# Kernel optimization log

Hardware: AMD Instinct MI355X
Metric: run time of the kernel (lower is better)

## Reference

```python
import jax, jax.numpy as jnp
import numpy as np

VERTICES = np.array([[-1.0, -1.0, 1.0], [-1.0, 1.0, 1.0], [1.0, 1.0, 1.0], [1.0, -1.0, 1.0]], dtype=np.float32)  # [4,3]


def _gather2d(img, yi, xi):
    # img: [C,IH,IW], yi/xi: [OH,OW] int32 -> [C,OH,OW]
    return img[:, yi, xi]


def _grid_sample_bilinear_zero(inp, grid):
    # inp: [B,C,IH,IW], grid: [B,OH,OW,2] in [-1,1] (x,y), align_corners=True (old torch semantics)
    B, C, IH, IW = inp.shape
    gx = grid[..., 0]
    gy = grid[..., 1]
    ix = (gx + 1.0) * (IW - 1) * 0.5
    iy = (gy + 1.0) * (IH - 1) * 0.5
    x0 = jnp.floor(ix)
    y0 = jnp.floor(iy)
    x1 = x0 + 1.0
    y1 = y0 + 1.0
    wx1 = ix - x0  # frac weights
    wy1 = iy - y0
    wx0 = 1.0 - wx1
    wy0 = 1.0 - wy1

    def corner(xf, yf, w):
        inb = ((xf >= 0) & (xf <= IW - 1) & (yf >= 0) & (yf <= IH - 1)).astype(inp.dtype)
        xi = jnp.clip(xf, 0, IW - 1).astype(jnp.int32)
        yi = jnp.clip(yf, 0, IH - 1).astype(jnp.int32)
        vals = jax.vmap(_gather2d)(inp, yi, xi)  # [B,C,OH,OW]
        return vals * (w * inb)[:, None, :, :]

    out = (corner(x0, y0, wx0 * wy0) + corner(x1, y0, wx1 * wy0)
           + corner(x0, y1, wx0 * wy1) + corner(x1, y1, wx1 * wy1))
    return out


def affine_spatial_transform(inp, theta, OH, OW):
    B, C, IH, IW = inp.shape
    hs = jnp.linspace(-1.0, 1.0, OH)
    ws = jnp.linspace(-1.0, 1.0, OW)
    hh = jnp.broadcast_to(hs[:, None], (OH, OW))
    ww = jnp.broadcast_to(ws[None, :], (OH, OW))
    t = jnp.stack([ww, hh, jnp.ones((OH, OW), dtype=inp.dtype)], axis=2)  # [OH,OW,3]
    # source_grid = theta @ t : [B,OH,OW,2]
    grid = jnp.einsum('bij,hwj->bhwi', theta, t)
    out = _grid_sample_bilinear_zero(inp, grid)
    v = jnp.asarray(VERTICES)  # [4,3]
    vout = jnp.einsum('bij,vj->bvi', theta, v)  # [B,4,2]
    x_coord = (vout[..., 0] + 1.0) * IW * 0.5
    y_coord = (vout[..., 1] + 1.0) * IH * 0.5
    vertices_out = jnp.stack([x_coord, y_coord], axis=2)  # [B,4,2]
    return out, vertices_out


def setup_inputs() -> dict:
    key = jax.random.key(0)
    k1, k2 = jax.random.split(key)
    B, C, IH, IW = 16, 64, 256, 256
    inp = jax.random.normal(k1, (B, C, IH, IW), dtype=jnp.float32)
    theta = jax.random.normal(k2, (B, 2, 3), dtype=jnp.float32)
    return {"input": inp, "theta": theta, "OH": 256, "OW": 256}


def reference(input, theta, OH, OW):
    return affine_spatial_transform(input, theta, OH, OW)
```

## Files before the change

kernel.cpp:

```cpp
#include <hip/hip_runtime.h>

#define B  16
#define C  64
#define IH 256
#define IW 256
#define OH 256
#define OW 256

#define TW 16
#define TH 16
#define CC 16
#define NWT (OW / TW)
#define NHT (OH / TH)
#define NCC (C / CC)
#define NB  (B * NCC * NHT * NWT)

typedef float f2 __attribute__((ext_vector_type(2)));
typedef f2 __attribute__((aligned(4))) f2u;

__global__ __launch_bounds__(256) void ast_fused(const float* __restrict__ inp,
                                                 const float* __restrict__ theta,
                                                 float* __restrict__ out) {
    if (blockIdx.x == 0 && threadIdx.x < B * 4) {
        const int tid = threadIdx.x;
        const int b = tid >> 2;
        const int v = tid & 3;
        const float vx_tab[4] = {-1.0f, -1.0f, 1.0f, 1.0f};
        const float vy_tab[4] = {-1.0f,  1.0f, 1.0f, -1.0f};
        const float Vx = vx_tab[v];
        const float Vy = vy_tab[v];
        const float ox = theta[b*6+0]*Vx + theta[b*6+1]*Vy + theta[b*6+2];
        const float oy = theta[b*6+3]*Vx + theta[b*6+4]*Vy + theta[b*6+5];
        float* vo = out + (size_t)B * C * OH * OW;
        vo[b*8 + v*2 + 0] = (ox + 1.0f) * ((float)IW * 0.5f);
        vo[b*8 + v*2 + 1] = (oy + 1.0f) * ((float)IH * 0.5f);
    }

    int id = (int)blockIdx.x;
    id = (id & 7) * (NB >> 3) + (id >> 3);

    const int wt = id & (NWT - 1); id >>= 4;
    const int ht = id & (NHT - 1); id >>= 4;
    const int b  = id & (B - 1);   id >>= 4;
    const int cc = id;

    const int tx = threadIdx.x & (TW - 1);
    const int ty = threadIdx.x >> 4;
    const int w = wt * TW + tx;
    const int h = ht * TH + ty;

    const float wn = -1.0f + (2.0f / (float)(OW - 1)) * (float)w;
    const float hn = -1.0f + (2.0f / (float)(OH - 1)) * (float)h;

    const float t00 = theta[b*6+0], t01 = theta[b*6+1], t02 = theta[b*6+2];
    const float t10 = theta[b*6+3], t11 = theta[b*6+4], t12 = theta[b*6+5];

    const float gx = t00 * wn + t01 * hn + t02;
    const float gy = t10 * wn + t11 * hn + t12;

    const float ix = (gx + 1.0f) * ((float)(IW - 1) * 0.5f);
    const float iy = (gy + 1.0f) * ((float)(IH - 1) * 0.5f);

    const float x0f = floorf(ix);
    const float y0f = floorf(iy);

    const float wx1 = ix - x0f;
    const float wy1 = iy - y0f;
    const float wx0 = 1.0f - wx1;
    const float wy0 = 1.0f - wy1;

    const bool inx0 = (x0f >= 0.0f) && (x0f <= (float)(IW - 1));
    const bool inx1 = (x0f + 1.0f >= 0.0f) && (x0f + 1.0f <= (float)(IW - 1));
    const bool iny0 = (y0f >= 0.0f) && (y0f <= (float)(IH - 1));
    const bool iny1 = (y0f + 1.0f >= 0.0f) && (y0f + 1.0f <= (float)(IH - 1));

    const float w00 = (inx0 && iny0) ? wx0 * wy0 : 0.0f;
    const float w10 = (inx1 && iny0) ? wx1 * wy0 : 0.0f;
    const float w01 = (inx0 && iny1) ? wx0 * wy1 : 0.0f;
    const float w11 = (inx1 && iny1) ? wx1 * wy1 : 0.0f;

    const int  basex = (int)fminf(fmaxf(x0f, 0.0f), (float)(IW - 2));
    const bool selA  = (x0f <= (float)(IW - 2));
    const bool selB  = (x0f >= 0.0f);

    const int y0 = (int)fminf(fmaxf(y0f,        0.0f), (float)(IH - 1));
    const int y1 = (int)fminf(fmaxf(y0f + 1.0f, 0.0f), (float)(IH - 1));

    const int off0 = y0 * IW + basex;
    const int off1 = y1 * IW + basex;

    const bool any_in = (inx0 || inx1) && (iny0 || iny1);

    const int c0 = cc * CC;
    const float* __restrict__ p = inp + ((size_t)b * C + c0) * (IH * IW);
    float* __restrict__ o = out + (((size_t)b * C + c0) * OH + h) * OW + w;

    if (any_in) {
        #pragma unroll 16
        for (int c = 0; c < CC; ++c) {
            const f2 ra = *(const f2u*)(p + off0);
            const f2 rb = *(const f2u*)(p + off1);
            const float a00 = selA ? ra.x : ra.y;
            const float a10 = selB ? ra.y : ra.x;
            const float b00 = selA ? rb.x : rb.y;
            const float b11 = selB ? rb.y : rb.x;
            float v = w00 * a00;
            v = fmaf(w10, a10, v);
            v = fmaf(w01, b00, v);
            v = fmaf(w11, b11, v);
            __builtin_nontemporal_store(v, o);
            p += IH * IW;
            o += OH * OW;
        }
    } else {
        #pragma unroll 16
        for (int c = 0; c < CC; ++c) {
            __builtin_nontemporal_store(0.0f, o);
            o += OH * OW;
        }
    }
}

extern "C" void kernel_launch(void* const* d_in, const int* in_sizes, int n_in,
                              void* d_out, int out_size, void* d_ws, size_t ws_size,
                              hipStream_t stream) {
    const float* inp   = (const float*)d_in[0];
    const float* theta = (const float*)d_in[1];
    float* out = (float*)d_out;

    ast_fused<<<NB, 256, 0, stream>>>(inp, theta, out);
}
```

Measured before the change: 495.9 us.

## Stage per-tile source bounding box in LDS across all channels with double buffering

Each block now covers one 16x16 output tile for all 64 channels. It computes the source-space bounding box of the tile's corners, cooperatively loads that box per channel into XOR-swizzled double-buffered shared memory with register prefetch of the next channel, and then does the bilinear gathers from LDS. Tiles whose box lies fully outside the image write zeros with an early return, and boxes too large for LDS fall back to direct global gathers. This is meant to replace scattered global gathers with coalesced loads, at the cost of one __syncthreads per channel, fewer blocks, and extra loads when the box is much larger than the tile footprint.

After: 609.1 us. +22.8%, slower.

```diff
diff --git a/kernel.cpp b/kernel.cpp
--- a/kernel.cpp
+++ b/kernel.cpp
@@ -9,61 +9,57 @@
 
 #define TW 16
 #define TH 16
-#define CC 16
 #define NWT (OW / TW)
 #define NHT (OH / TH)
-#define NCC (C / CC)
-#define NB  (B * NCC * NHT * NWT)
-
-typedef float f2 __attribute__((ext_vector_type(2)));
-typedef f2 __attribute__((aligned(4))) f2u;
+#define NB  (B * NHT * NWT)
+#define CAP 4096
+
+typedef float f4 __attribute__((ext_vector_type(4)));
 
 __global__ __launch_bounds__(256) void ast_fused(const float* __restrict__ inp,
                                                  const float* __restrict__ theta,
                                                  float* __restrict__ out) {
-    if (blockIdx.x == 0 && threadIdx.x < B * 4) {
-        const int tid = threadIdx.x;
-        const int b = tid >> 2;
-        const int v = tid & 3;
+    const int tid = threadIdx.x;
+
+    if (blockIdx.x == 0 && tid < B * 4) {
+        const int b_ = tid >> 2;
+        const int v  = tid & 3;
         const float vx_tab[4] = {-1.0f, -1.0f, 1.0f, 1.0f};
         const float vy_tab[4] = {-1.0f,  1.0f, 1.0f, -1.0f};
         const float Vx = vx_tab[v];
         const float Vy = vy_tab[v];
-        const float ox = theta[b*6+0]*Vx + theta[b*6+1]*Vy + theta[b*6+2];
-        const float oy = theta[b*6+3]*Vx + theta[b*6+4]*Vy + theta[b*6+5];
+        const float ox = theta[b_*6+0]*Vx + theta[b_*6+1]*Vy + theta[b_*6+2];
+        const float oy = theta[b_*6+3]*Vx + theta[b_*6+4]*Vy + theta[b_*6+5];
         float* vo = out + (size_t)B * C * OH * OW;
-        vo[b*8 + v*2 + 0] = (ox + 1.0f) * ((float)IW * 0.5f);
-        vo[b*8 + v*2 + 1] = (oy + 1.0f) * ((float)IH * 0.5f);
+        vo[b_*8 + v*2 + 0] = (ox + 1.0f) * ((float)IW * 0.5f);
+        vo[b_*8 + v*2 + 1] = (oy + 1.0f) * ((float)IH * 0.5f);
     }
 
     int id = (int)blockIdx.x;
     id = (id & 7) * (NB >> 3) + (id >> 3);
 
-    const int wt = id & (NWT - 1); id >>= 4;
-    const int ht = id & (NHT - 1); id >>= 4;
-    const int b  = id & (B - 1);   id >>= 4;
-    const int cc = id;
-
-    const int tx = threadIdx.x & (TW - 1);
-    const int ty = threadIdx.x >> 4;
+    const int wt = id & (NWT - 1);
+    const int ht = (id >> 4) & (NHT - 1);
+    const int b  = id >> 8;
+
+    const int tx = tid & (TW - 1);
+    const int ty = tid >> 4;
     const int w = wt * TW + tx;
     const int h = ht * TH + ty;
 
-    const float wn = -1.0f + (2.0f / (float)(OW - 1)) * (float)w;
-    const float hn = -1.0f + (2.0f / (float)(OH - 1)) * (float)h;
-
     const float t00 = theta[b*6+0], t01 = theta[b*6+1], t02 = theta[b*6+2];
     const float t10 = theta[b*6+3], t11 = theta[b*6+4], t12 = theta[b*6+5];
 
-    const float gx = t00 * wn + t01 * hn + t02;
-    const float gy = t10 * wn + t11 * hn + t12;
-
-    const float ix = (gx + 1.0f) * ((float)(IW - 1) * 0.5f);
-    const float iy = (gy + 1.0f) * ((float)(IH - 1) * 0.5f);
+    const float sWn = 2.0f / (float)(OW - 1);
+    const float sHn = 2.0f / (float)(OH - 1);
+
+    const float wn = -1.0f + sWn * (float)w;
+    const float hn = -1.0f + sHn * (float)h;
+    const float ix = (t00 * wn + t01 * hn + t02 + 1.0f) * ((float)(IW - 1) * 0.5f);
+    const float iy = (t10 * wn + t11 * hn + t12 + 1.0f) * ((float)(IH - 1) * 0.5f);
 
     const float x0f = floorf(ix);
     const float y0f = floorf(iy);
-
     const float wx1 = ix - x0f;
     const float wy1 = iy - y0f;
     const float wx0 = 1.0f - wx1;
@@ -79,45 +75,140 @@
     const float w01 = (inx0 && iny1) ? wx0 * wy1 : 0.0f;
     const float w11 = (inx1 && iny1) ? wx1 * wy1 : 0.0f;
 
-    const int  basex = (int)fminf(fmaxf(x0f, 0.0f), (float)(IW - 2));
-    const bool selA  = (x0f <= (float)(IW - 2));
-    const bool selB  = (x0f >= 0.0f);
-
-    const int y0 = (int)fminf(fmaxf(y0f,        0.0f), (float)(IH - 1));
-    const int y1 = (int)fminf(fmaxf(y0f + 1.0f, 0.0f), (float)(IH - 1));
-
-    const int off0 = y0 * IW + basex;
-    const int off1 = y1 * IW + basex;
-
-    const bool any_in = (inx0 || inx1) && (iny0 || iny1);
-
-    const int c0 = cc * CC;
-    const float* __restrict__ p = inp + ((size_t)b * C + c0) * (IH * IW);
-    float* __restrict__ o = out + (((size_t)b * C + c0) * OH + h) * OW + w;
-
-    if (any_in) {
-        #pragma unroll 16
-        for (int c = 0; c < CC; ++c) {
-            const f2 ra = *(const f2u*)(p + off0);
-            const f2 rb = *(const f2u*)(p + off1);
-            const float a00 = selA ? ra.x : ra.y;
-            const float a10 = selB ? ra.y : ra.x;
-            const float b00 = selA ? rb.x : rb.y;
-            const float b11 = selB ? rb.y : rb.x;
-            float v = w00 * a00;
-            v = fmaf(w10, a10, v);
-            v = fmaf(w01, b00, v);
-            v = fmaf(w11, b11, v);
-            __builtin_nontemporal_store(v, o);
-            p += IH * IW;
-            o += OH * OW;
-        }
-    } else {
-        #pragma unroll 16
-        for (int c = 0; c < CC; ++c) {
+    const float wnA = -1.0f + sWn * (float)(wt * TW);
+    const float wnB = -1.0f + sWn * (float)(wt * TW + TW - 1);
+    const float hnA = -1.0f + sHn * (float)(ht * TH);
+    const float hnB = -1.0f + sHn * (float)(ht * TH + TH - 1);
+
+    const float ixAA = (t00*wnA + t01*hnA + t02 + 1.0f) * 127.5f;
+    const float ixAB = (t00*wnA + t01*hnB + t02 + 1.0f) * 127.5f;
+    const float ixBA = (t00*wnB + t01*hnA + t02 + 1.0f) * 127.5f;
+    const float ixBB = (t00*wnB + t01*hnB + t02 + 1.0f) * 127.5f;
+    const float iyAA = (t10*wnA + t11*hnA + t12 + 1.0f) * 127.5f;
+    const float iyAB = (t10*wnA + t11*hnB + t12 + 1.0f) * 127.5f;
+    const float iyBA = (t10*wnB + t11*hnA + t12 + 1.0f) * 127.5f;
+    const float iyBB = (t10*wnB + t11*hnB + t12 + 1.0f) * 127.5f;
+
+    const float min_ix = fminf(fminf(ixAA, ixAB), fminf(ixBA, ixBB));
+    const float max_ix = fmaxf(fmaxf(ixAA, ixAB), fmaxf(ixBA, ixBB));
+    const float min_iy = fminf(fminf(iyAA, iyAB), fminf(iyBA, iyBB));
+    const float max_iy = fmaxf(fmaxf(iyAA, iyAB), fmaxf(iyBA, iyBB));
+
+    float* o = out + ((size_t)(b * C) << 16) + (size_t)(h * OW + w);
+
+    if (max_ix < -1.0f || min_ix > 256.0f || max_iy < -1.0f || min_iy > 256.0f) {
+        #pragma unroll 8
+        for (int c = 0; c < C; ++c) {
             __builtin_nontemporal_store(0.0f, o);
             o += OH * OW;
         }
+        return;
+    }
+
+    int bx0 = min(max((int)floorf(min_ix), 0), IW - 1);
+    int bx1 = min(min(max((int)floorf(max_ix), 0), IW - 1) + 1, IW - 1);
+    int by0 = min(max((int)floorf(min_iy), 0), IH - 1);
+    int by1 = min(min(max((int)floorf(max_iy), 0), IH - 1) + 1, IH - 1);
+    const int Wd = bx1 - bx0 + 1;
+    const int Hd = by1 - by0 + 1;
+    const int lw  = 32 - __builtin_clz((unsigned)max(Wd - 1, 3));
+    const int Wp  = 1 << lw;
+    const int msk = Wp - 1;
+    const int bx0p = min(bx0, IW - Wp);
+    const int HWp = Hd << lw;
+
+    const int x0i = (int)x0f;
+    const int y0i = (int)y0f;
+    const int x0c = min(max(x0i,     bx0), bx1);
+    const int x1c = min(max(x0i + 1, bx0), bx1);
+    const int y0c = min(max(y0i,     by0), by1);
+    const int y1c = min(max(y0i + 1, by0), by1);
+
+    const float* plane0 = inp + ((size_t)(b * C) << 16);
+
+    if (HWp > CAP) {
+        const int a00 = y0c * IW + x0c;
+        const int a01 = y0c * IW + x1c;
+        const int a10 = y1c * IW + x0c;
+        const int a11 = y1c * IW + x1c;
+        const float* pl = plane0;
+        for (int c = 0; c < C; ++c) {
+            float v = w00 * pl[a00];
+            v = fmaf(w10, pl[a01], v);
+            v = fmaf(w01, pl[a10], v);
+            v = fmaf(w11, pl[a11], v);
+            __builtin_nontemporal_store(v, o);
+            pl += IH * IW;
+            o  += OH * OW;
+        }
+        return;
+    }
+
+    const int xr0 = x0c - bx0p;
+    const int xr1 = x1c - bx0p;
+    const int r0  = y0c - by0;
+    const int r1  = y1c - by0;
+    const int o00 = (r0 << lw) + (xr0 ^ (r0 & msk));
+    const int o01 = (r0 << lw) + (xr1 ^ (r0 & msk));
+    const int o10 = (r1 << lw) + (xr0 ^ (r1 & msk));
+    const int o11 = (r1 << lw) + (xr1 ^ (r1 & msk));
+
+    int  ga[4][4];
+    bool act[4];
+    #pragma unroll
+    for (int g = 0; g < 4; ++g) {
+        const int i4 = g * 1024 + (tid << 2);
+        act[g] = (i4 < HWp);
+        const int r  = i4 >> lw;
+        const int xb = i4 & msk;
+        const int rowo = (by0 + r) * IW + bx0p;
+        const int rx = r & msk;
+        #pragma unroll
+        for (int j = 0; j < 4; ++j)
+            ga[g][j] = rowo + ((xb + j) ^ rx);
+    }
+
+    __shared__ float sb[2][CAP];
+
+    f4 pf[4];
+    #pragma unroll
+    for (int g = 0; g < 4; ++g) {
+        if (act[g]) {
+            pf[g].x = plane0[ga[g][0]];
+            pf[g].y = plane0[ga[g][1]];
+            pf[g].z = plane0[ga[g][2]];
+            pf[g].w = plane0[ga[g][3]];
+        }
+    }
+
+    #pragma unroll 2
+    for (int c = 0; c < C; ++c) {
+        const int cur = c & 1;
+        float* dst = &sb[cur][0];
+        #pragma unroll
+        for (int g = 0; g < 4; ++g) {
+            if (act[g]) *(f4*)&dst[g * 1024 + (tid << 2)] = pf[g];
+        }
+        if (c + 1 < C) {
+            const float* pl = plane0 + ((size_t)(c + 1) << 16);
+            #pragma unroll
+            for (int g = 0; g < 4; ++g) {
+                if (act[g]) {
+                    pf[g].x = pl[ga[g][0]];
+                    pf[g].y = pl[ga[g][1]];
+                    pf[g].z = pl[ga[g][2]];
+                    pf[g].w = pl[ga[g][3]];
+                }
+            }
+        }
+        __syncthreads();
+        const float* Lb = &sb[cur][0];
+        float v = w00 * Lb[o00];
+        v = fmaf(w10, Lb[o01], v);
+        v = fmaf(w01, Lb[o10], v);
+        v = fmaf(w11, Lb[o11], v);
+        __builtin_nontemporal_store(v, o);
+        o += OH * OW;
     }
 }
 
```
